# Kernel tuning notes

Measured on AMD Instinct MI355X. Metric: run time of the kernel, lower is better.

The kernel has to match this reference:

```python
import jax, jax.numpy as jnp
import numpy as np

B, SQ, SKV, D, H, DH = 4, 2048, 2048, 512, 8, 64  # inner_dim = H*DH = 512 = D
EPS = 1e-5


def layer_norm(x, g, b):
    mu = jnp.mean(x, axis=-1, keepdims=True)
    var = jnp.mean(jnp.square(x - mu), axis=-1, keepdims=True)
    return (x - mu) * jax.lax.rsqrt(var + EPS) * g + b


def setup_inputs() -> dict:
    key = jax.random.key(0)
    ks = jax.random.split(key, 8)
    s = 1.0 / np.sqrt(D)
    return {
        "x": jax.random.normal(ks[0], (B, SQ, D), jnp.float32),
        "y": jax.random.normal(ks[1], (B, SKV, D), jnp.float32),
        "ln_q_g": jnp.ones((D,), jnp.float32),
        "ln_q_b": jnp.zeros((D,), jnp.float32),
        "ln_kv_g": jnp.ones((D,), jnp.float32),
        "ln_kv_b": jnp.zeros((D,), jnp.float32),
        # weights stored [in, out] (transposed vs torch Linear.weight)
        "Wq": jax.random.normal(ks[2], (D, H * DH), jnp.float32) * s,
        "Wk": jax.random.normal(ks[3], (D, H * DH), jnp.float32) * s,
        "Wv": jax.random.normal(ks[4], (D, H * DH), jnp.float32) * s,
        "Wo": jax.random.normal(ks[5], (H * DH, D), jnp.float32) * s,
        "bo": jnp.zeros((D,), jnp.float32),
    }


def reference(x, y, ln_q_g, ln_q_b, ln_kv_g, ln_kv_b, Wq, Wk, Wv, Wo, bo):
    b, sq, _ = x.shape
    skv = y.shape[1]
    scale = DH ** -0.5
    xn = layer_norm(x, ln_q_g, ln_q_b)
    yn = layer_norm(y, ln_kv_g, ln_kv_b)
    q = (xn @ Wq).reshape(b, sq, H, DH).transpose(0, 2, 1, 3)   # b h sq dh
    k = (yn @ Wk).reshape(b, skv, H, DH).transpose(0, 2, 1, 3)  # b h skv dh
    v = (yn @ Wv).reshape(b, skv, H, DH).transpose(0, 2, 1, 3)
    dots = jnp.einsum("bhqd,bhkd->bhqk", q, k) * scale
    attn = jax.nn.softmax(dots, axis=-1)  # dropout is identity in eval / p=0
    out = jnp.einsum("bhqk,bhkd->bhqd", attn, v)
    out = out.transpose(0, 2, 1, 3).reshape(b, sq, H * DH)
    out = out @ Wo + bo
    return out, attn
```

## Files before the change

### kernel.cpp

```cpp
#include <hip/hip_runtime.h>

typedef float f32x4 __attribute__((ext_vector_type(4)));
typedef float f32x16 __attribute__((ext_vector_type(16)));
typedef __bf16 bf16x8 __attribute__((ext_vector_type(8)));
typedef short s16x8 __attribute__((ext_vector_type(8)));
typedef unsigned short u16;
typedef unsigned int u32;

#define DEV static __device__ __forceinline__

constexpr int BATCH = 4;
constexpr int SQ    = 2048;
constexpr int SKV   = 2048;
constexpr int DMODEL= 512;
constexpr int NH    = 8;
constexpr int DH    = 64;
constexpr int MROWS = BATCH * SQ;
constexpr float LN_EPS = 1e-5f;

DEV u16 f2bf(float f) {
    unsigned u = __builtin_bit_cast(unsigned, f);
    unsigned r = (u + 0x7FFFu + ((u >> 16) & 1u)) >> 16;
    return (u16)r;
}
DEV float bf2f(u16 h) { return __builtin_bit_cast(float, ((unsigned)h) << 16); }

DEV f32x4 mfma16(s16x8 a, s16x8 b, f32x4 c) {
    return __builtin_amdgcn_mfma_f32_16x16x32_bf16(
        __builtin_bit_cast(bf16x8, a), __builtin_bit_cast(bf16x8, b), c, 0, 0, 0);
}
DEV f32x16 mfma32(s16x8 a, s16x8 b, f32x16 c) {
    return __builtin_amdgcn_mfma_f32_32x32x16_bf16(
        __builtin_bit_cast(bf16x8, a), __builtin_bit_cast(bf16x8, b), c, 0, 0, 0);
}
DEV u32 cvtpk(float lo, float hi) {
    u32 r;
    asm("v_cvt_pk_bf16_f32 %0, %1, %2" : "=v"(r) : "v"(lo), "v"(hi));
    return r;
}

__global__ __launch_bounds__(256) void ln_kernel(
    const float* __restrict__ X, const float* __restrict__ G, const float* __restrict__ Bt,
    u16* __restrict__ oh)
{
    int row  = blockIdx.x * 4 + (threadIdx.x >> 6);
    int lane = threadIdx.x & 63;
    const float4* xr = (const float4*)(X + (size_t)row * DMODEL);
    float4 a = xr[lane * 2], b = xr[lane * 2 + 1];
    float vv[8] = {a.x, a.y, a.z, a.w, b.x, b.y, b.z, b.w};
    float s = 0.f;
#pragma unroll
    for (int i = 0; i < 8; i++) s += vv[i];
#pragma unroll
    for (int o = 32; o; o >>= 1) s += __shfl_xor(s, o);
    float mu = s * (1.0f / DMODEL);
    float vs = 0.f;
#pragma unroll
    for (int i = 0; i < 8; i++) { float d = vv[i] - mu; vs += d * d; }
#pragma unroll
    for (int o = 32; o; o >>= 1) vs += __shfl_xor(vs, o);
    float rstd = rsqrtf(vs * (1.0f / DMODEL) + LN_EPS);

    const float4* g4 = (const float4*)G;
    const float4* b4 = (const float4*)Bt;
    float4 g0 = g4[lane * 2], g1 = g4[lane * 2 + 1];
    float4 c0 = b4[lane * 2], c1 = b4[lane * 2 + 1];
    float gg[8] = {g0.x, g0.y, g0.z, g0.w, g1.x, g1.y, g1.z, g1.w};
    float cc[8] = {c0.x, c0.y, c0.z, c0.w, c1.x, c1.y, c1.z, c1.w};

    s16x8 vh;
#pragma unroll
    for (int i = 0; i < 8; i++) {
        float t = (vv[i] - mu) * rstd * gg[i] + cc[i];
        vh[i] = (short)f2bf(t);
    }
    *(s16x8*)(oh + (size_t)row * DMODEL + lane * 8) = vh;
}

__global__ __launch_bounds__(256) void wsplit_kernel(
    const float* __restrict__ W0, const float* __restrict__ W1,
    const float* __restrict__ W2, const float* __restrict__ W3,
    u16* __restrict__ t0)
{
    int which = blockIdx.y;
    const float* W = which == 0 ? W0 : which == 1 ? W1 : which == 2 ? W2 : W3;
    u16* th = t0 + (size_t)which * 262144;
    int idx = blockIdx.x * 256 + threadIdx.x;
    int n = idx >> 9, k = idx & 511;
    th[idx] = f2bf(W[(size_t)k * 512 + n]);
}

template<int MODE>
__global__ __launch_bounds__(256) void gemm_bf16(
    const u16* __restrict__ Ah, const u16* __restrict__ Bh,
    void* __restrict__ out0, const float* __restrict__ bias, float scl)
{
    constexpr int K  = 512;
    constexpr int LS = 72;
    __shared__ u16 lA[64][LS];
    __shared__ u16 lB[64][LS];

    int bm = blockIdx.x, bn = blockIdx.y;
    int tid = threadIdx.x, lane = tid & 63, wv = tid >> 6;
    int wm = (wv >> 1) * 32, wn = (wv & 1) * 32;
    int srow = tid >> 3, scol = (tid & 7) * 8;
    const size_t aoff0 = ((size_t)(bm * 64 + srow)) * K + scol;
    const size_t aoff1 = ((size_t)(bm * 64 + srow + 32)) * K + scol;
    const size_t boff0 = ((size_t)(bn * 64 + srow)) * K + scol;
    const size_t boff1 = ((size_t)(bn * 64 + srow + 32)) * K + scol;

    f32x4 acc[2][2] = {};

    for (int k0 = 0; k0 < K; k0 += 64) {
        *(int4*)&lA[srow][scol]      = *(const int4*)(Ah + aoff0 + k0);
        *(int4*)&lA[srow + 32][scol] = *(const int4*)(Ah + aoff1 + k0);
        *(int4*)&lB[srow][scol]      = *(const int4*)(Bh + boff0 + k0);
        *(int4*)&lB[srow + 32][scol] = *(const int4*)(Bh + boff1 + k0);
        __syncthreads();
        int fr = lane & 15, fg = (lane >> 4) * 8;
#pragma unroll
        for (int kk = 0; kk < 64; kk += 32) {
            s16x8 ah[2], bh[2];
#pragma unroll
            for (int m_ = 0; m_ < 2; m_++)
                ah[m_] = *(const s16x8*)&lA[wm + m_ * 16 + fr][kk + fg];
#pragma unroll
            for (int n_ = 0; n_ < 2; n_++)
                bh[n_] = *(const s16x8*)&lB[wn + n_ * 16 + fr][kk + fg];
#pragma unroll
            for (int m_ = 0; m_ < 2; m_++)
#pragma unroll
                for (int n_ = 0; n_ < 2; n_++)
                    acc[m_][n_] = mfma16(ah[m_], bh[n_], acc[m_][n_]);
        }
        __syncthreads();
    }

    int fr = lane & 15, fq = lane >> 4;
#pragma unroll
    for (int m_ = 0; m_ < 2; m_++)
#pragma unroll
        for (int n_ = 0; n_ < 2; n_++)
#pragma unroll
            for (int r = 0; r < 4; r++) {
                int gm = bm * 64 + wm + m_ * 16 + fq * 4 + r;
                int gn = bn * 64 + wn + n_ * 16 + fr;
                float v = acc[m_][n_][r];
                if (MODE == 6) {
                    v *= scl;
                    int b_ = gm >> 11, s_ = gm & 2047, h_ = gn >> 6, d_ = gn & 63;
                    size_t adr = (((size_t)(b_ * NH + h_)) * SKV + s_) * DH + d_;
                    ((u16*)out0)[adr] = f2bf(v);
                } else if (MODE == 5) {
                    int b_ = gm >> 11, s_ = gm & 2047, h_ = gn >> 6, d_ = gn & 63;
                    size_t adr = (((size_t)(b_ * NH + h_)) * DH + d_) * SKV + s_;
                    ((u16*)out0)[adr] = f2bf(v);
                } else {
                    v += bias[gn];
                    ((float*)out0)[(size_t)gm * DMODEL + gn] = v;
                }
            }
}

__global__ __launch_bounds__(256, 4) void attn_kernel(
    const u16* __restrict__ Qh, const u16* __restrict__ Kh,
    const u16* __restrict__ VT,
    float* __restrict__ attn, u16* __restrict__ ch)
{
    __shared__ float R[4][2112];
    __shared__ float rs[4][32];
    int tid = threadIdx.x, lane = tid & 63, wid = tid >> 6;
    int h  = lane >> 5;
    int ql = lane & 31;
    int off = 8 * h;

    int vb = (blockIdx.x & 7) * 256 + (blockIdx.x >> 3);
    int bh = vb >> 6;
    int qt = vb & 63;
    int q0 = qt * 32;
    const size_t base = (size_t)bh * (SKV * DH);
    int kt0 = wid * 16;

    s16x8 qf[4];
    {
        const u16* qp = Qh + base + ((size_t)(q0 + ql)) * DH + off;
#pragma unroll
        for (int c = 0; c < 4; c++) qf[c] = *(const s16x8*)(qp + c * 16);
    }

    float rsum0 = 0.f, rsum1 = 0.f;
    for (int kt = kt0; kt < kt0 + 16; kt++) {
        size_t kb = base + ((size_t)(kt * 32 + ql)) * DH + off;
        s16x8 kh[4];
#pragma unroll
        for (int c = 0; c < 4; c++) kh[c] = *(const s16x8*)(Kh + kb + c * 16);
        f32x16 a1 = 0;
#pragma unroll
        for (int c = 0; c < 4; c++) a1 = mfma32(kh[c], qf[c], a1);
#pragma unroll
        for (int r = 0; r < 16; r += 2) {
            rsum0 += __expf(a1[r]);
            rsum1 += __expf(a1[r + 1]);
        }
    }
    float rsum = rsum0 + rsum1;
    rsum += __shfl_xor(rsum, 32);
    if (lane < 32) rs[wid][ql] = rsum;
    __syncthreads();
    float inv_l = 1.0f / (rs[0][ql] + rs[1][ql] + rs[2][ql] + rs[3][ql]);

    f32x16 pv0 = 0, pv1 = 0;
    const u16* vbase = VT + (size_t)bh * (DH * SKV) + (size_t)ql * SKV + off;

    s16x8 kA[4];
    {
        size_t kb = base + ((size_t)(kt0 * 32 + ql)) * DH + off;
#pragma unroll
        for (int c = 0; c < 4; c++) kA[c] = *(const s16x8*)(Kh + kb + c * 16);
    }

    for (int i = 0; i < 16; i++) {
        int kt = kt0 + i;
        const u16* vp = vbase + kt * 32;
        s16x8 v00 = *(const s16x8*)(vp);
        s16x8 v01 = *(const s16x8*)(vp + 16);
        s16x8 v10 = *(const s16x8*)(vp + (size_t)32 * SKV);
        s16x8 v11 = *(const s16x8*)(vp + (size_t)32 * SKV + 16);
        s16x8 kB[4];
        if (i + 1 < 16) {
            size_t kb = base + ((size_t)((kt + 1) * 32 + ql)) * DH + off;
#pragma unroll
            for (int c = 0; c < 4; c++) kB[c] = *(const s16x8*)(Kh + kb + c * 16);
        }
        f32x16 acc = 0;
#pragma unroll
        for (int c = 0; c < 4; c++) acc = mfma32(kA[c], qf[c], acc);
#pragma unroll
        for (int r = 0; r < 16; r++) acc[r] = __expf(acc[r]) * inv_l;

        u32 O0[4], O1[4];
#pragma unroll
        for (int g = 0; g < 4; g++) {
            O0[g] = cvtpk(acc[4 * g + 0], acc[4 * g + 1]);
            O1[g] = cvtpk(acc[4 * g + 2], acc[4 * g + 3]);
        }
        {
            u32 a = O0[0], b = O0[1], c = O1[0], d = O1[1];
            asm("v_permlane32_swap_b32 %0, %1" : "+v"(a), "+v"(b));
            asm("v_permlane32_swap_b32 %0, %1" : "+v"(c), "+v"(d));
            uint4 w = {a, c, b, d};
            s16x8 bf = __builtin_bit_cast(s16x8, w);
            pv0 = mfma32(v00, bf, pv0);
            pv1 = mfma32(v10, bf, pv1);
        }
        {
            u32 a = O0[2], b = O0[3], c = O1[2], d = O1[3];
            asm("v_permlane32_swap_b32 %0, %1" : "+v"(a), "+v"(b));
            asm("v_permlane32_swap_b32 %0, %1" : "+v"(c), "+v"(d));
            uint4 w = {a, c, b, d};
            s16x8 bf = __builtin_bit_cast(s16x8, w);
            pv0 = mfma32(v01, bf, pv0);
            pv1 = mfma32(v11, bf, pv1);
        }

        float* buf = &R[wid][(i & 1) * 1056];
#pragma unroll
        for (int r = 0; r < 16; r++)
            buf[ql * 33 + (r & 3) + 8 * (r >> 2) + 4 * h] = acc[r];

#pragma unroll
        for (int p = 0; p < 4; p++) {
            int q = p * 8 + (lane >> 3), j4 = (lane & 7) * 4;
            f32x4 o;
            o.x = buf[q * 33 + j4 + 0];
            o.y = buf[q * 33 + j4 + 1];
            o.z = buf[q * 33 + j4 + 2];
            o.w = buf[q * 33 + j4 + 3];
            __builtin_nontemporal_store(o,
                (f32x4*)&attn[((size_t)(bh * SQ + q0 + q)) * SKV + kt * 32 + j4]);
        }

#pragma unroll
        for (int c = 0; c < 4; c++) kA[c] = kB[c];
    }

#pragma unroll
    for (int r = 0; r < 16; r++) {
        R[wid][r * 64 + lane]        = pv0[r];
        R[wid][1024 + r * 64 + lane] = pv1[r];
    }
    __syncthreads();

    if (wid < 2) {
        int X = wid;
        float s[16];
#pragma unroll
        for (int r = 0; r < 16; r++)
            s[r] = R[0][X * 1024 + r * 64 + lane] + R[1][X * 1024 + r * 64 + lane]
                 + R[2][X * 1024 + r * 64 + lane] + R[3][X * 1024 + r * 64 + lane];
        int b_ = bh >> 3, hh = bh & 7;
        size_t rowa = ((size_t)(b_ * SQ + q0 + ql)) * DMODEL + hh * 64 + X * 32 + 4 * h;
#pragma unroll
        for (int g = 0; g < 4; g++) {
            u16 hv[4];
#pragma unroll
            for (int i = 0; i < 4; i++) hv[i] = f2bf(s[4 * g + i]);
            *(ushort4*)(ch + rowa + 8 * g) = *(ushort4*)hv;
        }
    }
}

extern "C" void kernel_launch(void* const* d_in, const int* in_sizes, int n_in,
                              void* d_out, int out_size, void* d_ws, size_t ws_size,
                              hipStream_t stream)
{
    const float* x   = (const float*)d_in[0];
    const float* y   = (const float*)d_in[1];
    const float* lqg = (const float*)d_in[2];
    const float* lqb = (const float*)d_in[3];
    const float* lkg = (const float*)d_in[4];
    const float* lkb = (const float*)d_in[5];
    const float* Wq  = (const float*)d_in[6];
    const float* Wk  = (const float*)d_in[7];
    const float* Wv  = (const float*)d_in[8];
    const float* Wo  = (const float*)d_in[9];
    const float* bo  = (const float*)d_in[10];

    char* ws = (char*)d_ws;
    size_t off = 0;
    auto alloc = [&](size_t nelem) -> u16* {
        u16* p = (u16*)(ws + off);
        off += (nelem * 2 + 255) & ~(size_t)255;
        return p;
    };
    const size_t NROW = (size_t)MROWS * DMODEL;
    u16* xnh = alloc(NROW);
    u16* ynh = alloc(NROW);
    u16* wbase = alloc(4 * 262144);
    u16* wqh = wbase + 0 * 262144;
    u16* wkh = wbase + 1 * 262144;
    u16* wvh = wbase + 2 * 262144;
    u16* woh = wbase + 3 * 262144;
    u16* qh_ = alloc(NROW);
    u16* kh_ = alloc(NROW);
    u16* vt_ = alloc(NROW);
    u16* ct_ = alloc(NROW);

    float* outp  = (float*)d_out;
    float* attnp = outp + (size_t)MROWS * DMODEL;

    ln_kernel<<<MROWS / 4, 256, 0, stream>>>(x, lqg, lqb, xnh);
    ln_kernel<<<MROWS / 4, 256, 0, stream>>>(y, lkg, lkb, ynh);
    wsplit_kernel<<<dim3(1024, 4), 256, 0, stream>>>(Wq, Wk, Wv, Wo, wbase);

    dim3 gg(MROWS / 64, 512 / 64);
    gemm_bf16<6><<<gg, 256, 0, stream>>>(xnh, wqh, qh_, nullptr, 0.125f);
    gemm_bf16<6><<<gg, 256, 0, stream>>>(ynh, wkh, kh_, nullptr, 1.0f);
    gemm_bf16<5><<<gg, 256, 0, stream>>>(ynh, wvh, vt_, nullptr, 1.0f);

    attn_kernel<<<2048, 256, 0, stream>>>(qh_, kh_, vt_, attnp, ct_);

    gemm_bf16<4><<<gg, 256, 0, stream>>>(ct_, woh, (void*)outp, bo, 1.0f);
}
```

Baseline: 260.4 us.

## Fuse K and V projection GEMMs and fold log2e into Q scale for exp2

Replaces the separate K and V projection GEMM launches with one kernel that loads each normalized-Y tile once and computes both K and transposed V from it, halving the A-operand traffic and saving a launch. It also folds log2(e) into the Q scaling so the attention kernel can use the hardware exp2 instruction directly instead of __expf. The fused kernel uses more shared memory and accumulator registers, which may lower occupancy. The transposed V stores remain scattered.

```diff
diff --git a/kernel.cpp b/kernel.cpp
--- a/kernel.cpp
+++ b/kernel.cpp
@@ -17,6 +17,7 @@
 constexpr int DH    = 64;
 constexpr int MROWS = BATCH * SQ;
 constexpr float LN_EPS = 1e-5f;
+constexpr float LOG2E  = 1.44269504088896340736f;
 
 DEV u16 f2bf(float f) {
     unsigned u = __builtin_bit_cast(unsigned, f);
@@ -24,6 +25,7 @@
     return (u16)r;
 }
 DEV float bf2f(u16 h) { return __builtin_bit_cast(float, ((unsigned)h) << 16); }
+DEV float exp2fast(float x) { return __builtin_amdgcn_exp2f(x); }
 
 DEV f32x4 mfma16(s16x8 a, s16x8 b, f32x4 c) {
     return __builtin_amdgcn_mfma_f32_16x16x32_bf16(
@@ -151,14 +153,79 @@
                     int b_ = gm >> 11, s_ = gm & 2047, h_ = gn >> 6, d_ = gn & 63;
                     size_t adr = (((size_t)(b_ * NH + h_)) * SKV + s_) * DH + d_;
                     ((u16*)out0)[adr] = f2bf(v);
-                } else if (MODE == 5) {
-                    int b_ = gm >> 11, s_ = gm & 2047, h_ = gn >> 6, d_ = gn & 63;
-                    size_t adr = (((size_t)(b_ * NH + h_)) * DH + d_) * SKV + s_;
-                    ((u16*)out0)[adr] = f2bf(v);
                 } else {
                     v += bias[gn];
                     ((float*)out0)[(size_t)gm * DMODEL + gn] = v;
                 }
+            }
+}
+
+__global__ __launch_bounds__(256) void gemm_kv(
+    const u16* __restrict__ Ah, const u16* __restrict__ Bk, const u16* __restrict__ Bv,
+    u16* __restrict__ outK, u16* __restrict__ outVT)
+{
+    constexpr int K  = 512;
+    constexpr int LS = 72;
+    __shared__ u16 lA[64][LS];
+    __shared__ u16 lK[64][LS];
+    __shared__ u16 lV[64][LS];
+
+    int bm = blockIdx.x, bn = blockIdx.y;
+    int tid = threadIdx.x, lane = tid & 63, wv = tid >> 6;
+    int wm = (wv >> 1) * 32, wn = (wv & 1) * 32;
+    int srow = tid >> 3, scol = (tid & 7) * 8;
+    const size_t aoff0 = ((size_t)(bm * 64 + srow)) * K + scol;
+    const size_t aoff1 = ((size_t)(bm * 64 + srow + 32)) * K + scol;
+    const size_t boff0 = ((size_t)(bn * 64 + srow)) * K + scol;
+    const size_t boff1 = ((size_t)(bn * 64 + srow + 32)) * K + scol;
+
+    f32x4 ak[2][2] = {}, av[2][2] = {};
+
+    for (int k0 = 0; k0 < K; k0 += 64) {
+        *(int4*)&lA[srow][scol]      = *(const int4*)(Ah + aoff0 + k0);
+        *(int4*)&lA[srow + 32][scol] = *(const int4*)(Ah + aoff1 + k0);
+        *(int4*)&lK[srow][scol]      = *(const int4*)(Bk + boff0 + k0);
+        *(int4*)&lK[srow + 32][scol] = *(const int4*)(Bk + boff1 + k0);
+        *(int4*)&lV[srow][scol]      = *(const int4*)(Bv + boff0 + k0);
+        *(int4*)&lV[srow + 32][scol] = *(const int4*)(Bv + boff1 + k0);
+        __syncthreads();
+        int fr = lane & 15, fg = (lane >> 4) * 8;
+#pragma unroll
+        for (int kk = 0; kk < 64; kk += 32) {
+            s16x8 af[2], bk[2], bv[2];
+#pragma unroll
+            for (int m_ = 0; m_ < 2; m_++)
+                af[m_] = *(const s16x8*)&lA[wm + m_ * 16 + fr][kk + fg];
+#pragma unroll
+            for (int n_ = 0; n_ < 2; n_++) {
+                bk[n_] = *(const s16x8*)&lK[wn + n_ * 16 + fr][kk + fg];
+                bv[n_] = *(const s16x8*)&lV[wn + n_ * 16 + fr][kk + fg];
+            }
+#pragma unroll
+            for (int m_ = 0; m_ < 2; m_++)
+#pragma unroll
+                for (int n_ = 0; n_ < 2; n_++) {
+                    ak[m_][n_] = mfma16(af[m_], bk[n_], ak[m_][n_]);
+                    av[m_][n_] = mfma16(af[m_], bv[n_], av[m_][n_]);
+                }
+        }
+        __syncthreads();
+    }
+
+    int fr = lane & 15, fq = lane >> 4;
+#pragma unroll
+    for (int m_ = 0; m_ < 2; m_++)
+#pragma unroll
+        for (int n_ = 0; n_ < 2; n_++)
+#pragma unroll
+            for (int r = 0; r < 4; r++) {
+                int gm = bm * 64 + wm + m_ * 16 + fq * 4 + r;
+                int gn = bn * 64 + wn + n_ * 16 + fr;
+                int b_ = gm >> 11, s_ = gm & 2047, h_ = gn >> 6, d_ = gn & 63;
+                size_t adrK = (((size_t)(b_ * NH + h_)) * SKV + s_) * DH + d_;
+                size_t adrV = (((size_t)(b_ * NH + h_)) * DH + d_) * SKV + s_;
+                outK[adrK]  = f2bf(ak[m_][n_][r]);
+                outVT[adrV] = f2bf(av[m_][n_][r]);
             }
 }
 
@@ -199,8 +266,8 @@
         for (int c = 0; c < 4; c++) a1 = mfma32(kh[c], qf[c], a1);
 #pragma unroll
         for (int r = 0; r < 16; r += 2) {
-            rsum0 += __expf(a1[r]);
-            rsum1 += __expf(a1[r + 1]);
+            rsum0 += exp2fast(a1[r]);
+            rsum1 += exp2fast(a1[r + 1]);
         }
     }
     float rsum = rsum0 + rsum1;
@@ -236,7 +303,7 @@
 #pragma unroll
         for (int c = 0; c < 4; c++) acc = mfma32(kA[c], qf[c], acc);
 #pragma unroll
-        for (int r = 0; r < 16; r++) acc[r] = __expf(acc[r]) * inv_l;
+        for (int r = 0; r < 16; r++) acc[r] = exp2fast(acc[r]) * inv_l;
 
         u32 O0[4], O1[4];
 #pragma unroll
@@ -354,9 +421,8 @@
     wsplit_kernel<<<dim3(1024, 4), 256, 0, stream>>>(Wq, Wk, Wv, Wo, wbase);
 
     dim3 gg(MROWS / 64, 512 / 64);
-    gemm_bf16<6><<<gg, 256, 0, stream>>>(xnh, wqh, qh_, nullptr, 0.125f);
-    gemm_bf16<6><<<gg, 256, 0, stream>>>(ynh, wkh, kh_, nullptr, 1.0f);
-    gemm_bf16<5><<<gg, 256, 0, stream>>>(ynh, wvh, vt_, nullptr, 1.0f);
+    gemm_bf16<6><<<gg, 256, 0, stream>>>(xnh, wqh, qh_, nullptr, 0.125f * LOG2E);
+    gemm_kv<<<gg, 256, 0, stream>>>(ynh, wkh, wvh, kh_, vt_);
 
     attn_kernel<<<2048, 256, 0, stream>>>(qh_, kh_, vt_, attnp, ct_);
 
```

After: 254.6 us. 2.2% less time.
